# Optimization experiments

Measured on AMD Instinct MI355X. Metric: run time of the kernel, lower is better.

The kernel has to match this reference:

```python
import jax, jax.numpy as jnp
import numpy as np

N = 8192          # num nodes
E = 262144        # num edges (avg degree 32)
IN = 128          # in_channels
HID = 64          # hidden_channels
H = 4             # heads (conv1)
OUT = 16          # out_channels
THRESH = 0.5      # distance threshold for adjacency rebuild
SLOPE = 0.2       # PyG GATConv negative_slope default


def setup_inputs() -> dict:
    key = jax.random.key(0)
    ks = jax.random.split(key, 10)
    s = 0.1
    return {
        "x": jax.random.normal(ks[0], (N, IN), jnp.float32),
        "edge_index": jax.random.randint(ks[1], (2, E), 0, N, dtype=jnp.int64),
        # conv1 params (GATConv in->hid, heads=H, concat=True)
        "W1": jax.random.normal(ks[2], (IN, H * HID), jnp.float32) * s,
        "att_src1": jax.random.normal(ks[3], (H, HID), jnp.float32) * s,
        "att_dst1": jax.random.normal(ks[4], (H, HID), jnp.float32) * s,
        "b1": jax.random.normal(ks[5], (H * HID,), jnp.float32) * s,
        # conv2 params (GATConv H*hid->out, heads=1, concat=False)
        "W2": jax.random.normal(ks[6], (H * HID, OUT), jnp.float32) * s,
        "att_src2": jax.random.normal(ks[7], (OUT,), jnp.float32) * s,
        "att_dst2": jax.random.normal(ks[8], (OUT,), jnp.float32) * s,
        "b2": jax.random.normal(ks[9], (OUT,), jnp.float32) * s,
    }


def reference(x, edge_index, W1, att_src1, att_dst1, b1, W2, att_src2, att_dst2, b2):
    n = x.shape[0]
    # ---- conv1: sparse edge-wise GAT (gather -> segment-softmax -> scatter) ----
    h = (x @ W1).reshape(n, H, HID)                         # [N,H,C]
    loops = jnp.arange(n, dtype=edge_index.dtype)           # PyG adds self-loops
    src = jnp.concatenate([edge_index[0], loops])
    dst = jnp.concatenate([edge_index[1], loops])
    a_s = jnp.sum(h * att_src1, axis=-1)                    # [N,H]
    a_d = jnp.sum(h * att_dst1, axis=-1)                    # [N,H]
    e = jax.nn.leaky_relu(a_s[src] + a_d[dst], SLOPE)       # [E+N,H]
    emax = jax.ops.segment_max(e, dst, num_segments=n)      # stable softmax per dst
    ez = jnp.exp(e - emax[dst])
    denom = jax.ops.segment_sum(ez, dst, num_segments=n)
    alpha = ez / denom[dst]                                 # [E+N,H]
    agg = jax.ops.segment_sum(h[src] * alpha[..., None], dst, num_segments=n)
    h1 = jax.nn.elu(agg.reshape(n, H * HID) + b1)           # [N, H*HID]

    # ---- adjacency rebuild: pairwise Euclidean distance + threshold (detached) ----
    f = jax.lax.stop_gradient(h1)                           # torch .detach()
    sq = jnp.sum(f * f, axis=-1)                            # [N]
    d2 = sq[:, None] + sq[None, :] - 2.0 * (f @ f.T)        # squared distances
    dist = jnp.sqrt(jnp.maximum(d2, 0.0))
    adj = dist < THRESH                                     # [N,N], symmetric, self incl.

    # ---- conv2: dense masked GAT attention over rebuilt adjacency (heads=1) ----
    h2 = h1 @ W2                                            # [N,OUT]
    s2 = h2 @ att_src2                                      # [N] (source term)
    t2 = h2 @ att_dst2                                      # [N] (target term)
    # edge j->i exists iff adj[i,j]; score[i,j] = leaky_relu(a_src.h2[j] + a_dst.h2[i])
    scores = jax.nn.leaky_relu(s2[None, :] + t2[:, None], SLOPE)
    scores = jnp.where(adj, scores, -jnp.inf)
    alpha2 = jax.nn.softmax(scores, axis=1)                 # softmax over neighbors j
    out = alpha2 @ h2 + b2                                  # [N,OUT]
    return jax.nn.log_softmax(out, axis=1)
```

## Files before the change

### kernel.cpp

```cpp
#include <hip/hip_runtime.h>
#include <hip/hip_bf16.h>
#include <math.h>

#define NN 8192
#define NE 262144
#define EA (NE + NN)
#define SLOPE 0.2f
#define TH2 0.25f

typedef __bf16 bf16x8 __attribute__((ext_vector_type(8)));
typedef float f32x16 __attribute__((ext_vector_type(16)));

__device__ __forceinline__ float lrelu(float x) { return x > 0.f ? x : SLOPE * x; }

__device__ __forceinline__ void gl_lds16(const void* g, void* l) {
  __builtin_amdgcn_global_load_lds((const __attribute__((address_space(1))) void*)g,
                                   (__attribute__((address_space(3))) void*)l, 16, 0, 0);
}

__global__ void k_gemm1(const float* __restrict__ x, const float* __restrict__ W1,
                        const float* __restrict__ as1, const float* __restrict__ ad1,
                        float* __restrict__ h, float* __restrict__ a_s,
                        float* __restrict__ a_d) {
  const int nb = blockIdx.x << 2;
  const int t = threadIdx.x;
  __shared__ float xs[4][128];
  if (t < 128) ((float4*)xs)[t] = ((const float4*)(x + (size_t)nb * 128))[t];
  __syncthreads();
  float ac[4] = {0.f, 0.f, 0.f, 0.f};
  const float* wp = W1 + t;
#pragma unroll 4
  for (int k = 0; k < 128; ++k) {
    float wv = wp[(size_t)k << 8];
    ac[0] = fmaf(xs[0][k], wv, ac[0]);
    ac[1] = fmaf(xs[1][k], wv, ac[1]);
    ac[2] = fmaf(xs[2][k], wv, ac[2]);
    ac[3] = fmaf(xs[3][k], wv, ac[3]);
  }
  const float as1t = as1[t], ad1t = ad1[t];
#pragma unroll
  for (int i = 0; i < 4; ++i) {
    h[((size_t)(nb + i) << 8) + t] = ac[i];
    float av = ac[i] * as1t;
    float dv = ac[i] * ad1t;
#pragma unroll
    for (int m = 32; m >= 1; m >>= 1) {
      av += __shfl_xor(av, m, 64);
      dv += __shfl_xor(dv, m, 64);
    }
    if ((t & 63) == 0) {
      a_s[((nb + i) << 2) + (t >> 6)] = av;
      a_d[((nb + i) << 2) + (t >> 6)] = dv;
    }
  }
}

__global__ void k_init(int* __restrict__ cnt) {
  int i = blockIdx.x * 256 + threadIdx.x;
  if (i < NN) cnt[i] = 1;
}
__global__ void k_hist(const int* __restrict__ ei, int* __restrict__ cnt) {
  int e = blockIdx.x * 256 + threadIdx.x;
  if (e < NE) atomicAdd(&cnt[ei[NE + e]], 1);
}
__global__ void k_scan(const int* __restrict__ cnt, int* __restrict__ start,
                       int* __restrict__ cursor) {
  __shared__ int s[1024];
  const int t = threadIdx.x;
  const int base = t << 3;
  int c[8];
  int run = 0;
#pragma unroll
  for (int i = 0; i < 8; ++i) { c[i] = cnt[base + i]; run += c[i]; }
  s[t] = run;
  __syncthreads();
  const int total = run;
  for (int off = 1; off < 1024; off <<= 1) {
    int v = (t >= off) ? s[t - off] : 0;
    __syncthreads();
    s[t] += v;
    __syncthreads();
  }
  int o = s[t] - total;
#pragma unroll
  for (int i = 0; i < 8; ++i) {
    start[base + i] = o;
    cursor[base + i] = o;
    o += c[i];
  }
}
__global__ void k_scatter(const int* __restrict__ ei, int* __restrict__ cursor,
                          int* __restrict__ eidx) {
  int e = blockIdx.x * 256 + threadIdx.x;
  if (e >= EA) return;
  int src, dst;
  if (e < NE) { src = ei[e]; dst = ei[NE + e]; } else { src = dst = e - NE; }
  int slot = atomicAdd(&cursor[dst], 1);
  eidx[slot] = src;
}

__global__ void k_node(const int* __restrict__ start, const int* __restrict__ cnt,
                       const int* __restrict__ eidx, const float* __restrict__ a_s,
                       const float* __restrict__ a_d, const float* __restrict__ h,
                       const float* __restrict__ b1, const float* __restrict__ W2,
                       const float* __restrict__ as2, const float* __restrict__ ad2,
                       __bf16* __restrict__ fbf, float* __restrict__ sq,
                       float2* __restrict__ jsg, float* __restrict__ t2g,
                       float* __restrict__ h2g) {
  const int n = blockIdx.x, t = threadIdx.x;
  __shared__ float red[16];
  __shared__ float hl[256];
  __shared__ float r2[4];
  __shared__ float h2l[16];
  const int st = start[n];
  const int deg = cnt[n];
  const float4 ad4 = *(const float4*)(a_d + ((size_t)n << 2));
  float pm0 = -INFINITY, pm1 = -INFINITY, pm2 = -INFINITY, pm3 = -INFINITY;
  for (int e = t; e < deg; e += 256) {
    int src = eidx[st + e];
    float4 s4 = *(const float4*)(a_s + ((size_t)src << 2));
    pm0 = fmaxf(pm0, lrelu(s4.x + ad4.x));
    pm1 = fmaxf(pm1, lrelu(s4.y + ad4.y));
    pm2 = fmaxf(pm2, lrelu(s4.z + ad4.z));
    pm3 = fmaxf(pm3, lrelu(s4.w + ad4.w));
  }
#pragma unroll
  for (int m = 32; m >= 1; m >>= 1) {
    pm0 = fmaxf(pm0, __shfl_xor(pm0, m, 64));
    pm1 = fmaxf(pm1, __shfl_xor(pm1, m, 64));
    pm2 = fmaxf(pm2, __shfl_xor(pm2, m, 64));
    pm3 = fmaxf(pm3, __shfl_xor(pm3, m, 64));
  }
  if ((t & 63) == 0) {
    const int w = t >> 6;
    red[(w << 2) + 0] = pm0;
    red[(w << 2) + 1] = pm1;
    red[(w << 2) + 2] = pm2;
    red[(w << 2) + 3] = pm3;
  }
  __syncthreads();
  const int hd = t >> 6;
  const float mhead = fmaxf(fmaxf(red[0 + hd], red[4 + hd]),
                            fmaxf(red[8 + hd], red[12 + hd]));
  const float adh = (hd == 0) ? ad4.x : (hd == 1) ? ad4.y : (hd == 2) ? ad4.z : ad4.w;
  float den = 0.f, acc = 0.f;
  for (int e = 0; e < deg; ++e) {
    int src = eidx[st + e];
    float av = a_s[((size_t)src << 2) + hd];
    float ez = __expf(lrelu(av + adh) - mhead);
    den += ez;
    acc = fmaf(ez, h[((size_t)src << 8) + t], acc);
  }
  float v = acc / den + b1[t];
  float h1 = v > 0.f ? v : (__expf(v) - 1.f);
  fbf[((size_t)n << 8) + t] = (__bf16)h1;
  hl[t] = h1;
  float s = h1 * h1;
#pragma unroll
  for (int m = 32; m >= 1; m >>= 1) s += __shfl_xor(s, m, 64);
  if ((t & 63) == 0) r2[t >> 6] = s;
  __syncthreads();
  if (t < 16) {
    float a = 0.f;
#pragma unroll 8
    for (int c = 0; c < 256; ++c) a = fmaf(hl[c], W2[(c << 4) + t], a);
    h2g[((size_t)n << 4) + t] = a;
    h2l[t] = a;
  }
  __syncthreads();
  if (t == 0) {
    float sqv = r2[0] + r2[1] + r2[2] + r2[3];
    sq[n] = sqv;
    float ss = 0.f;
#pragma unroll
    for (int o = 0; o < 16; ++o) ss += h2l[o] * as2[o];
    jsg[n] = make_float2((sqv - TH2) * 0.5f, ss);
  } else if (t == 1) {
    float tt = 0.f;
#pragma unroll
    for (int o = 0; o < 16; ++o) tt += h2l[o] * ad2[o];
    t2g[n] = tt;
  }
}

__launch_bounds__(256, 1)
__global__ void k_conv2(const __bf16* __restrict__ fbf, const float* __restrict__ sq,
                        const float2* __restrict__ jsg, const float* __restrict__ t2g,
                        const float* __restrict__ h2g, const float* __restrict__ b2,
                        float* __restrict__ out) {
  __shared__ __align__(16) char fjl[2][65536];
  __shared__ float thrl[2][128];
  __shared__ float s2l[2][128];
  __shared__ float mrg[256][18];

  const int t = threadIdx.x;
  const int lane = t & 63;
  const int w = t >> 6;
  const int half = lane >> 5;
  const int rowA = lane & 31;
  const int i0 = blockIdx.x << 5;
  const int jw = w << 5;

  bf16x8 bfr[16];
  {
    const char* fb = (const char*)fbf + (((size_t)(i0 + rowA)) << 9) + (half << 4);
#pragma unroll
    for (int kc = 0; kc < 16; ++kc) bfr[kc] = *(const bf16x8*)(fb + kc * 32);
  }
  const float sqi = sq[i0 + rowA];
  const float t2i = t2g[i0 + rowA];
  const float gbase = 0.5f * sqi;

  float m = -INFINITY, l = 0.f;
  float o[16];
#pragma unroll
  for (int c = 0; c < 16; ++c) o[c] = 0.f;

#define STAGE(B, JT)                                                                   \
  do {                                                                                 \
    const size_t j0b = ((size_t)(JT)) << 7;                                            \
    _Pragma("unroll") for (int p = 0; p < 16; ++p) {                                   \
      const int r0 = p * 8 + (w << 1);                                                 \
      const int r = r0 + half;                                                         \
      const int cb = (lane & 31) << 4;                                                 \
      const char* src =                                                                \
          (const char*)fbf + ((j0b + r) << 9) + (cb ^ ((r & 31) << 4));                \
      gl_lds16(src, (void*)(fjl[B] + (r0 << 9)));                                      \
    }                                                                                  \
    if (t < 128) {                                                                     \
      float2 v = jsg[j0b + t];                                                         \
      thrl[B][t] = v.x;                                                                \
      s2l[B][t] = v.y;                                                                 \
    }                                                                                  \
  } while (0)

  STAGE(0, 0);
  __syncthreads();
  int cur = 0;

  for (int jt = 0; jt < 64; ++jt) {
    if (jt < 63) STAGE(cur ^ 1, jt + 1);

    f32x16 acc0, acc1;
#pragma unroll
    for (int r = 0; r < 16; ++r) { acc0[r] = 0.f; acc1[r] = 0.f; }
    const char* fjrow = fjl[cur] + ((size_t)(jw + rowA) << 9);
    const int ksw = half << 4;
    const int rsw = rowA << 4;
#pragma unroll
    for (int kc = 0; kc < 16; kc += 2) {
      bf16x8 a0 = *(const bf16x8*)(fjrow + ((kc * 32 + ksw) ^ rsw));
      bf16x8 a1 = *(const bf16x8*)(fjrow + (((kc + 1) * 32 + ksw) ^ rsw));
      acc0 = __builtin_amdgcn_mfma_f32_32x32x16_bf16(a0, bfr[kc], acc0, 0, 0, 0);
      acc1 = __builtin_amdgcn_mfma_f32_32x32x16_bf16(a1, bfr[kc + 1], acc1, 0, 0, 0);
    }

    const float* tb = thrl[cur] + jw + (half << 2);
    const float* sb = s2l[cur] + jw + (half << 2);
    float4 th0 = *(const float4*)(tb + 0);
    float4 th1 = *(const float4*)(tb + 8);
    float4 th2 = *(const float4*)(tb + 16);
    float4 th3 = *(const float4*)(tb + 24);
    float4 sv0 = *(const float4*)(sb + 0);
    float4 sv1 = *(const float4*)(sb + 8);
    float4 sv2 = *(const float4*)(sb + 16);
    float4 sv3 = *(const float4*)(sb + 24);
    const float thv[16] = {th0.x, th0.y, th0.z, th0.w, th1.x, th1.y, th1.z, th1.w,
                           th2.x, th2.y, th2.z, th2.w, th3.x, th3.y, th3.z, th3.w};
    const float s2v[16] = {sv0.x, sv0.y, sv0.z, sv0.w, sv1.x, sv1.y, sv1.z, sv1.w,
                           sv2.x, sv2.y, sv2.z, sv2.w, sv3.x, sv3.y, sv3.z, sv3.w};

    unsigned msk = 0;
#pragma unroll
    for (int r = 0; r < 16; ++r) {
      float g = acc0[r] + acc1[r];
      if (g > gbase + thv[r]) msk |= (1u << r);
    }

    if (msk) {
      const int j0 = (jt << 7) + jw + (half << 2);
#pragma unroll
      for (int r = 0; r < 16; ++r) {
        if (msk & (1u << r)) {
          float e = lrelu(s2v[r] + t2i);
          if (e > m) {
            float scl = __expf(m - e);
            l *= scl;
#pragma unroll
            for (int c = 0; c < 16; ++c) o[c] *= scl;
            m = e;
          }
          float p = __expf(e - m);
          l += p;
          int j = j0 + (r & 3) + ((r >> 2) << 3);
          const float4* hp = (const float4*)(h2g + ((size_t)j << 4));
          float4 q0 = hp[0], q1 = hp[1], q2 = hp[2], q3 = hp[3];
          o[0] += p * q0.x;  o[1] += p * q0.y;  o[2] += p * q0.z;  o[3] += p * q0.w;
          o[4] += p * q1.x;  o[5] += p * q1.y;  o[6] += p * q1.z;  o[7] += p * q1.w;
          o[8] += p * q2.x;  o[9] += p * q2.y;  o[10] += p * q2.z; o[11] += p * q2.w;
          o[12] += p * q3.x; o[13] += p * q3.y; o[14] += p * q3.z; o[15] += p * q3.w;
        }
      }
    }
    __syncthreads();
    cur ^= 1;
  }

  {
    float* mp = mrg[(w << 6) + lane];
    mp[0] = m;
    mp[1] = l;
#pragma unroll
    for (int c = 0; c < 16; ++c) mp[2 + c] = o[c];
  }
  __syncthreads();
  if (t < 32) {
    float M = -INFINITY;
#pragma unroll
    for (int s = 0; s < 8; ++s)
      M = fmaxf(M, mrg[((s >> 1) << 6) + ((s & 1) << 5) + t][0]);
    float L = 0.f, O[16];
#pragma unroll
    for (int c = 0; c < 16; ++c) O[c] = 0.f;
#pragma unroll
    for (int s = 0; s < 8; ++s) {
      const float* mp = mrg[((s >> 1) << 6) + ((s & 1) << 5) + t];
      float wt = __expf(mp[0] - M);
      L += mp[1] * wt;
#pragma unroll
      for (int c = 0; c < 16; ++c) O[c] += mp[2 + c] * wt;
    }
    float inv = 1.f / L;
    float v[16];
    float mx = -INFINITY;
#pragma unroll
    for (int c = 0; c < 16; ++c) {
      v[c] = O[c] * inv + b2[c];
      mx = fmaxf(mx, v[c]);
    }
    float se = 0.f;
#pragma unroll
    for (int c = 0; c < 16; ++c) se += __expf(v[c] - mx);
    float lse = mx + __logf(se);
    float4* op = (float4*)(out + ((size_t)(i0 + t) << 4));
#pragma unroll
    for (int gq = 0; gq < 4; ++gq)
      op[gq] = make_float4(v[gq * 4 + 0] - lse, v[gq * 4 + 1] - lse,
                           v[gq * 4 + 2] - lse, v[gq * 4 + 3] - lse);
  }
#undef STAGE
}

extern "C" void kernel_launch(void* const* d_in, const int* in_sizes, int n_in,
                              void* d_out, int out_size, void* d_ws, size_t ws_size,
                              hipStream_t stream) {
  const float* x   = (const float*)d_in[0];
  const int*   ei  = (const int*)d_in[1];
  const float* W1  = (const float*)d_in[2];
  const float* as1 = (const float*)d_in[3];
  const float* ad1 = (const float*)d_in[4];
  const float* b1  = (const float*)d_in[5];
  const float* W2  = (const float*)d_in[6];
  const float* as2 = (const float*)d_in[7];
  const float* ad2 = (const float*)d_in[8];
  const float* b2  = (const float*)d_in[9];
  float* out = (float*)d_out;

  float* p = (float*)d_ws;
  float* h    = p; p += (size_t)NN * 256;
  float* a_s  = p; p += (size_t)NN * 4;
  float* a_d  = p; p += (size_t)NN * 4;
  float* sq   = p; p += NN;
  float* t2   = p; p += NN;
  float* h2g  = p; p += (size_t)NN * 16;
  float2* jsg = (float2*)p; p += (size_t)NN * 2;
  __bf16* fbf = (__bf16*)p; p += (size_t)NN * 128;
  int* cnt    = (int*)p; p += NN;
  int* startp = (int*)p; p += NN;
  int* cursor = (int*)p; p += NN;
  int* eidx   = (int*)p;

  k_init<<<NN / 256, 256, 0, stream>>>(cnt);
  k_hist<<<NE / 256, 256, 0, stream>>>(ei, cnt);
  k_gemm1<<<NN / 4, 256, 0, stream>>>(x, W1, as1, ad1, h, a_s, a_d);
  k_scan<<<1, 1024, 0, stream>>>(cnt, startp, cursor);
  k_scatter<<<(EA + 255) / 256, 256, 0, stream>>>(ei, cursor, eidx);
  k_node<<<NN, 256, 0, stream>>>(startp, cnt, eidx, a_s, a_d, h, b1, W2, as2, ad2,
                                 fbf, sq, jsg, t2, h2g);
  k_conv2<<<NN / 32, 256, 0, stream>>>(fbf, sq, jsg, t2, h2g, b2, out);
}
```

Before: 311.4 us.

## Give each wave private LDS buffers in conv2 and drop block barriers

Each wave in the dense conv2 kernel now stages its own 32-row slice of neighbour features plus threshold and source-score values into a private double-buffered LDS region. It waits on outstanding loads with explicit vmcnt waits, so the per-tile __syncthreads is gone. The aim is to stop waves stalling on each other while keeping loads overlapped with MFMA. The threshold and score arrays are split into separate float arrays so they can be copied straight to LDS with 4-byte direct loads. Separately, the k_node edge loop is unrolled by four with independent accumulators to expose more memory-level parallelism. The hand-counted vmcnt(20) is fragile if the compiler reorders or adds loads, and the larger LDS pool must still fit in one block.

```diff
diff --git a/kernel.cpp b/kernel.cpp
--- a/kernel.cpp
+++ b/kernel.cpp
@@ -16,6 +16,10 @@
 __device__ __forceinline__ void gl_lds16(const void* g, void* l) {
   __builtin_amdgcn_global_load_lds((const __attribute__((address_space(1))) void*)g,
                                    (__attribute__((address_space(3))) void*)l, 16, 0, 0);
+}
+__device__ __forceinline__ void gl_lds4(const void* g, void* l) {
+  __builtin_amdgcn_global_load_lds((const __attribute__((address_space(1))) void*)g,
+                                   (__attribute__((address_space(3))) void*)l, 4, 0, 0);
 }
 
 __global__ void k_gemm1(const float* __restrict__ x, const float* __restrict__ W1,
@@ -105,8 +109,8 @@
                        const float* __restrict__ b1, const float* __restrict__ W2,
                        const float* __restrict__ as2, const float* __restrict__ ad2,
                        __bf16* __restrict__ fbf, float* __restrict__ sq,
-                       float2* __restrict__ jsg, float* __restrict__ t2g,
-                       float* __restrict__ h2g) {
+                       float* __restrict__ thr_g, float* __restrict__ s2_g,
+                       float* __restrict__ t2g, float* __restrict__ h2g) {
   const int n = blockIdx.x, t = threadIdx.x;
   __shared__ float red[16];
   __shared__ float hl[256];
@@ -143,14 +147,30 @@
   const float mhead = fmaxf(fmaxf(red[0 + hd], red[4 + hd]),
                             fmaxf(red[8 + hd], red[12 + hd]));
   const float adh = (hd == 0) ? ad4.x : (hd == 1) ? ad4.y : (hd == 2) ? ad4.z : ad4.w;
-  float den = 0.f, acc = 0.f;
-  for (int e = 0; e < deg; ++e) {
-    int src = eidx[st + e];
-    float av = a_s[((size_t)src << 2) + hd];
-    float ez = __expf(lrelu(av + adh) - mhead);
-    den += ez;
-    acc = fmaf(ez, h[((size_t)src << 8) + t], acc);
-  }
+  float dn0 = 0.f, dn1 = 0.f, dn2 = 0.f, dn3 = 0.f;
+  float ac0 = 0.f, ac1 = 0.f, ac2 = 0.f, ac3 = 0.f;
+  int e = 0;
+  for (; e + 3 < deg; e += 4) {
+    int s0 = eidx[st + e + 0], s1 = eidx[st + e + 1];
+    int s2i = eidx[st + e + 2], s3 = eidx[st + e + 3];
+    float z0 = __expf(lrelu(a_s[((size_t)s0 << 2) + hd] + adh) - mhead);
+    float z1 = __expf(lrelu(a_s[((size_t)s1 << 2) + hd] + adh) - mhead);
+    float z2 = __expf(lrelu(a_s[((size_t)s2i << 2) + hd] + adh) - mhead);
+    float z3 = __expf(lrelu(a_s[((size_t)s3 << 2) + hd] + adh) - mhead);
+    dn0 += z0; dn1 += z1; dn2 += z2; dn3 += z3;
+    ac0 = fmaf(z0, h[((size_t)s0 << 8) + t], ac0);
+    ac1 = fmaf(z1, h[((size_t)s1 << 8) + t], ac1);
+    ac2 = fmaf(z2, h[((size_t)s2i << 8) + t], ac2);
+    ac3 = fmaf(z3, h[((size_t)s3 << 8) + t], ac3);
+  }
+  for (; e < deg; ++e) {
+    int s0 = eidx[st + e];
+    float z0 = __expf(lrelu(a_s[((size_t)s0 << 2) + hd] + adh) - mhead);
+    dn0 += z0;
+    ac0 = fmaf(z0, h[((size_t)s0 << 8) + t], ac0);
+  }
+  float den = (dn0 + dn1) + (dn2 + dn3);
+  float acc = (ac0 + ac1) + (ac2 + ac3);
   float v = acc / den + b1[t];
   float h1 = v > 0.f ? v : (__expf(v) - 1.f);
   fbf[((size_t)n << 8) + t] = (__bf16)h1;
@@ -174,7 +194,8 @@
     float ss = 0.f;
 #pragma unroll
     for (int o = 0; o < 16; ++o) ss += h2l[o] * as2[o];
-    jsg[n] = make_float2((sqv - TH2) * 0.5f, ss);
+    thr_g[n] = (sqv - TH2) * 0.5f;
+    s2_g[n] = ss;
   } else if (t == 1) {
     float tt = 0.f;
 #pragma unroll
@@ -185,21 +206,31 @@
 
 __launch_bounds__(256, 1)
 __global__ void k_conv2(const __bf16* __restrict__ fbf, const float* __restrict__ sq,
-                        const float2* __restrict__ jsg, const float* __restrict__ t2g,
-                        const float* __restrict__ h2g, const float* __restrict__ b2,
-                        float* __restrict__ out) {
-  __shared__ __align__(16) char fjl[2][65536];
-  __shared__ float thrl[2][128];
-  __shared__ float s2l[2][128];
-  __shared__ float mrg[256][18];
+                        const float* __restrict__ thr_g, const float* __restrict__ s2_g,
+                        const float* __restrict__ t2g, const float* __restrict__ h2g,
+                        const float* __restrict__ b2, float* __restrict__ out) {
+  __shared__ __align__(16) char pool[139264];
 
   const int t = threadIdx.x;
   const int lane = t & 63;
   const int w = t >> 6;
   const int half = lane >> 5;
-  const int rowA = lane & 31;
+  const int lo = lane & 31;
+  const int rowA = lo;
   const int i0 = blockIdx.x << 5;
   const int jw = w << 5;
+  char* wbase = pool + w * 34816;
+
+  int stoff[16];
+#pragma unroll
+  for (int p = 0; p < 16; ++p) {
+    int rw = (p << 1) + half;
+    stoff[p] = ((jw + rw) << 9) + (((lo ^ rw) & 31) << 4);
+  }
+  int colkey[16];
+#pragma unroll
+  for (int kc = 0; kc < 16; ++kc)
+    colkey[kc] = ((((kc << 1) + half) ^ rowA) & 31) << 4;
 
   bf16x8 bfr[16];
   {
@@ -209,72 +240,71 @@
   }
   const float sqi = sq[i0 + rowA];
   const float t2i = t2g[i0 + rowA];
-  const float gbase = 0.5f * sqi;
+  const float gb_i = 0.5f * sqi;
 
   float m = -INFINITY, l = 0.f;
   float o[16];
 #pragma unroll
   for (int c = 0; c < 16; ++c) o[c] = 0.f;
 
-#define STAGE(B, JT)                                                                   \
-  do {                                                                                 \
-    const size_t j0b = ((size_t)(JT)) << 7;                                            \
-    _Pragma("unroll") for (int p = 0; p < 16; ++p) {                                   \
-      const int r0 = p * 8 + (w << 1);                                                 \
-      const int r = r0 + half;                                                         \
-      const int cb = (lane & 31) << 4;                                                 \
-      const char* src =                                                                \
-          (const char*)fbf + ((j0b + r) << 9) + (cb ^ ((r & 31) << 4));                \
-      gl_lds16(src, (void*)(fjl[B] + (r0 << 9)));                                      \
-    }                                                                                  \
-    if (t < 128) {                                                                     \
-      float2 v = jsg[j0b + t];                                                         \
-      thrl[B][t] = v.x;                                                                \
-      s2l[B][t] = v.y;                                                                 \
-    }                                                                                  \
+#define STAGE(B, JT)                                                        \
+  do {                                                                      \
+    const char* gsrc = (const char*)fbf + ((size_t)(JT) << 16);             \
+    char* lb_ = wbase + (B)*17408;                                          \
+    _Pragma("unroll") for (int p = 0; p < 16; ++p)                          \
+        gl_lds16(gsrc + stoff[p], lb_ + (p << 10));                         \
+    gl_lds4(thr_g + ((JT) << 7) + lane, lb_ + 16384);                       \
+    gl_lds4(thr_g + ((JT) << 7) + 64 + lane, lb_ + 16384 + 256);            \
+    gl_lds4(s2_g + ((JT) << 7) + lane, lb_ + 16896);                        \
+    gl_lds4(s2_g + ((JT) << 7) + 64 + lane, lb_ + 16896 + 256);             \
   } while (0)
 
   STAGE(0, 0);
-  __syncthreads();
-  int cur = 0;
 
   for (int jt = 0; jt < 64; ++jt) {
-    if (jt < 63) STAGE(cur ^ 1, jt + 1);
+    const int cur = jt & 1;
+    if (jt < 63) {
+      STAGE(cur ^ 1, jt + 1);
+      asm volatile("s_waitcnt vmcnt(20)" ::: "memory");
+    } else {
+      asm volatile("s_waitcnt vmcnt(0)" ::: "memory");
+    }
+    char* lb = wbase + cur * 17408;
+    const char* rb = lb + (rowA << 9);
 
     f32x16 acc0, acc1;
 #pragma unroll
     for (int r = 0; r < 16; ++r) { acc0[r] = 0.f; acc1[r] = 0.f; }
-    const char* fjrow = fjl[cur] + ((size_t)(jw + rowA) << 9);
-    const int ksw = half << 4;
-    const int rsw = rowA << 4;
 #pragma unroll
     for (int kc = 0; kc < 16; kc += 2) {
-      bf16x8 a0 = *(const bf16x8*)(fjrow + ((kc * 32 + ksw) ^ rsw));
-      bf16x8 a1 = *(const bf16x8*)(fjrow + (((kc + 1) * 32 + ksw) ^ rsw));
+      bf16x8 a0 = *(const bf16x8*)(rb + colkey[kc]);
+      bf16x8 a1 = *(const bf16x8*)(rb + colkey[kc + 1]);
       acc0 = __builtin_amdgcn_mfma_f32_32x32x16_bf16(a0, bfr[kc], acc0, 0, 0, 0);
       acc1 = __builtin_amdgcn_mfma_f32_32x32x16_bf16(a1, bfr[kc + 1], acc1, 0, 0, 0);
     }
 
-    const float* tb = thrl[cur] + jw + (half << 2);
-    const float* sb = s2l[cur] + jw + (half << 2);
-    float4 th0 = *(const float4*)(tb + 0);
-    float4 th1 = *(const float4*)(tb + 8);
-    float4 th2 = *(const float4*)(tb + 16);
-    float4 th3 = *(const float4*)(tb + 24);
-    float4 sv0 = *(const float4*)(sb + 0);
-    float4 sv1 = *(const float4*)(sb + 8);
-    float4 sv2 = *(const float4*)(sb + 16);
-    float4 sv3 = *(const float4*)(sb + 24);
-    const float thv[16] = {th0.x, th0.y, th0.z, th0.w, th1.x, th1.y, th1.z, th1.w,
-                           th2.x, th2.y, th2.z, th2.w, th3.x, th3.y, th3.z, th3.w};
-    const float s2v[16] = {sv0.x, sv0.y, sv0.z, sv0.w, sv1.x, sv1.y, sv1.z, sv1.w,
-                           sv2.x, sv2.y, sv2.z, sv2.w, sv3.x, sv3.y, sv3.z, sv3.w};
+    const float* thp = (const float*)(lb + 16384);
+    const float* s2p = (const float*)(lb + 16896);
+    float4 thq[4], s2q[4];
+#pragma unroll
+    for (int q = 0; q < 4; ++q) {
+      thq[q] = *(const float4*)(thp + jw + (half << 2) + (q << 3));
+      s2q[q] = *(const float4*)(s2p + jw + (half << 2) + (q << 3));
+    }
+    const float thv[16] = {thq[0].x, thq[0].y, thq[0].z, thq[0].w,
+                           thq[1].x, thq[1].y, thq[1].z, thq[1].w,
+                           thq[2].x, thq[2].y, thq[2].z, thq[2].w,
+                           thq[3].x, thq[3].y, thq[3].z, thq[3].w};
+    const float s2v[16] = {s2q[0].x, s2q[0].y, s2q[0].z, s2q[0].w,
+                           s2q[1].x, s2q[1].y, s2q[1].z, s2q[1].w,
+                           s2q[2].x, s2q[2].y, s2q[2].z, s2q[2].w,
+                           s2q[3].x, s2q[3].y, s2q[3].z, s2q[3].w};
 
     unsigned msk = 0;
 #pragma unroll
     for (int r = 0; r < 16; ++r) {
       float g = acc0[r] + acc1[r];
-      if (g > gbase + thv[r]) msk |= (1u << r);
+      if (g > gb_i + thv[r]) msk |= (1u << r);
     }
 
     if (msk) {
@@ -302,12 +332,12 @@
         }
       }
     }
-    __syncthreads();
-    cur ^= 1;
-  }
-
+  }
+
+  __syncthreads();
+  float (*mrg)[18] = (float(*)[18])pool;
   {
-    float* mp = mrg[(w << 6) + lane];
+    float* mp = mrg[t];
     mp[0] = m;
     mp[1] = l;
 #pragma unroll
@@ -367,18 +397,19 @@
   float* out = (float*)d_out;
 
   float* p = (float*)d_ws;
-  float* h    = p; p += (size_t)NN * 256;
-  float* a_s  = p; p += (size_t)NN * 4;
-  float* a_d  = p; p += (size_t)NN * 4;
-  float* sq   = p; p += NN;
-  float* t2   = p; p += NN;
-  float* h2g  = p; p += (size_t)NN * 16;
-  float2* jsg = (float2*)p; p += (size_t)NN * 2;
-  __bf16* fbf = (__bf16*)p; p += (size_t)NN * 128;
-  int* cnt    = (int*)p; p += NN;
-  int* startp = (int*)p; p += NN;
-  int* cursor = (int*)p; p += NN;
-  int* eidx   = (int*)p;
+  float* h     = p; p += (size_t)NN * 256;
+  float* a_s   = p; p += (size_t)NN * 4;
+  float* a_d   = p; p += (size_t)NN * 4;
+  float* sq    = p; p += NN;
+  float* t2    = p; p += NN;
+  float* h2g   = p; p += (size_t)NN * 16;
+  float* thr_g = p; p += NN;
+  float* s2_g  = p; p += NN;
+  __bf16* fbf  = (__bf16*)p; p += (size_t)NN * 128;
+  int* cnt     = (int*)p; p += NN;
+  int* startp  = (int*)p; p += NN;
+  int* cursor  = (int*)p; p += NN;
+  int* eidx    = (int*)p;
 
   k_init<<<NN / 256, 256, 0, stream>>>(cnt);
   k_hist<<<NE / 256, 256, 0, stream>>>(ei, cnt);
@@ -386,6 +417,6 @@
   k_scan<<<1, 1024, 0, stream>>>(cnt, startp, cursor);
   k_scatter<<<(EA + 255) / 256, 256, 0, stream>>>(ei, cursor, eidx);
   k_node<<<NN, 256, 0, stream>>>(startp, cnt, eidx, a_s, a_d, h, b1, W2, as2, ad2,
-                                 fbf, sq, jsg, t2, h2g);
-  k_conv2<<<NN / 32, 256, 0, stream>>>(fbf, sq, jsg, t2, h2g, b2, out);
-}
+                                 fbf, sq, thr_g, s2_g, t2, h2g);
+  k_conv2<<<NN / 32, 256, 0, stream>>>(fbf, sq, thr_g, s2_g, t2, h2g, b2, out);
+}
```

Measured after the change: 261.4 us. -16.1%, faster.
